# Kernel tuning notes

Measured on AMD Instinct MI355X. Metric: run time of the kernel, lower is better.

Reference implementation:

```python
import jax, jax.numpy as jnp
import numpy as np

N, E, D, G, OUT, K = 150000, 1200000, 128, 512, 2, 2
EPS = 1e-5


def setup_inputs() -> dict:
    key = jax.random.key(0)
    ks = jax.random.split(key, 8)
    nfeat = jax.random.normal(ks[0], (N, D), dtype=jnp.float32)
    src = jax.random.randint(ks[1], (E,), 0, N, dtype=jnp.int32)
    dst = jax.random.randint(ks[2], (E,), 0, N, dtype=jnp.int32)
    node2graph = jnp.sort(jax.random.randint(ks[3], (N,), 0, G, dtype=jnp.int32))
    s = 1.0 / np.sqrt(D)
    conv_w = jax.random.normal(ks[4], (D, D), dtype=jnp.float32) * s
    conv_b = jnp.zeros((D,), jnp.float32)
    gamma1 = jnp.ones((D,), jnp.float32)
    beta1 = jnp.zeros((D,), jnp.float32)
    gamma2 = jnp.ones((D,), jnp.float32)
    beta2 = jnp.zeros((D,), jnp.float32)
    pred_w = jax.random.normal(ks[5], (D, OUT), dtype=jnp.float32) * s
    pred_b = jnp.zeros((OUT,), jnp.float32)
    return {"nfeat": nfeat, "src": src, "dst": dst, "node2graph": node2graph,
            "num_graphs": G,
            "conv_w": conv_w, "conv_b": conv_b,
            "gamma1": gamma1, "beta1": beta1,
            "gamma2": gamma2, "beta2": beta2,
            "pred_w": pred_w, "pred_b": pred_b}


def _batchnorm(h, gamma, beta):
    # batch-norm over the node dimension (training-mode stats)
    mu = jnp.mean(h, axis=0)
    var = jnp.mean(jnp.square(h - mu), axis=0)
    return (h - mu) * jax.lax.rsqrt(var + EPS) * gamma + beta


def reference(nfeat, src, dst, node2graph, num_graphs,
              conv_w, conv_b, gamma1, beta1, gamma2, beta2, pred_w, pred_b):
    n = nfeat.shape[0]
    # symmetric degree normalization D^{-1/2} A D^{-1/2}
    deg = jax.ops.segment_sum(jnp.ones_like(dst, dtype=nfeat.dtype), dst, num_segments=n)
    dnorm = jax.lax.rsqrt(jnp.clip(deg, 1.0, None))  # [N]
    h = nfeat  # dropout with p=0 is identity
    for _ in range(K):  # k-hop SGC propagation interleaved with norm
        m = (h * dnorm[:, None])[src]                       # [E, D] gather
        h = jax.ops.segment_sum(m, dst, num_segments=n)     # scatter-add
        h = h * dnorm[:, None]
        h = _batchnorm(h, gamma1, beta1)
    h = h @ conv_w + conv_b          # SGConv linear
    h = _batchnorm(h, gamma2, beta2)  # middle norm
    h = jax.nn.relu(h)                # activation (dropout p=0)
    # mean pooling per graph
    cnt = jax.ops.segment_sum(jnp.ones((n,), h.dtype), node2graph, num_segments=num_graphs)
    g = jax.ops.segment_sum(h, node2graph, num_segments=num_graphs)
    g = g / jnp.clip(cnt, 1.0, None)[:, None]
    return g @ pred_w + pred_b  # [G, OUT]
```

## Files before the change

### kernel.cpp

```cpp
#include <hip/hip_runtime.h>
#include <hip/hip_fp16.h>
#include <cstddef>
#include <cstdint>

constexpr int DIMS = 128;
constexpr float BN_EPS = 1e-5f;
constexpr int NSH = 64;
constexpr int GB = 4096;
constexpr int NPB = 512;

typedef _Float16 f16x8 __attribute__((ext_vector_type(8)));
typedef float f32x4 __attribute__((ext_vector_type(4)));

static __device__ __forceinline__ f16x8 as_f16x8(uint4 u) {
  union { uint4 u; f16x8 h; } x; x.u = u; return x.h;
}
static __device__ __forceinline__ __half2 as_h2(uint32_t u) {
  union { uint32_t u; __half2 h; } x; x.u = u; return x.h;
}

__global__ void zero_k(float* __restrict__ fp, size_t nf) {
  size_t i = (size_t)blockIdx.x * blockDim.x + threadIdx.x;
  if (i < nf) fp[i] = 0.f;
}

__global__ void cvt_k(const float* __restrict__ in, uint32_t* __restrict__ out,
                      const float* __restrict__ dnorm, size_t n64) {
  size_t i = (size_t)blockIdx.x * blockDim.x + threadIdx.x;
  size_t stride = (size_t)gridDim.x * blockDim.x;
  const float2* in2 = (const float2*)in;
  for (; i < n64; i += stride) {
    float d = dnorm[i >> 6];
    float2 v = in2[i];
    __half2 h = __floats2half2_rn(v.x * d, v.y * d);
    out[i] = *(const uint32_t*)&h;
  }
}


__global__ __launch_bounds__(256) void cnt_k(const int* __restrict__ dst,
                                             int* __restrict__ C, int e, int chunk) {
  __shared__ int hist[512];
  int b = blockIdx.x;
  for (int j = threadIdx.x; j < 512; j += 256) hist[j] = 0;
  __syncthreads();
  int i0 = b * chunk;
  int i1 = i0 + chunk; if (i1 > e) i1 = e;
  for (int i = i0 + threadIdx.x; i < i1; i += 256)
    atomicAdd(&hist[dst[i] >> 9], 1);
  __syncthreads();
  for (int j = threadIdx.x; j < 512; j += 256) C[b * 512 + j] = hist[j];
}

__global__ __launch_bounds__(512) void colscan_k(int* __restrict__ C, int* __restrict__ tot) {
  int j = blockIdx.x;
  int t = threadIdx.x;
  int v = C[t * 512 + j];
  __shared__ int lds[512];
  lds[t] = v; __syncthreads();
  for (int off = 1; off < 512; off <<= 1) {
    int add = (t >= off) ? lds[t - off] : 0;
    __syncthreads();
    lds[t] += add;
    __syncthreads();
  }
  C[t * 512 + j] = lds[t] - v;
  if (t == 511) tot[j] = lds[511];
}

__global__ __launch_bounds__(512) void bscan_k(const int* __restrict__ tot, int nbins,
                                               int* __restrict__ boff, int e) {
  int t = threadIdx.x;
  int v = tot[t];
  __shared__ int lds[512];
  lds[t] = v; __syncthreads();
  for (int off = 1; off < 512; off <<= 1) {
    int add = (t >= off) ? lds[t - off] : 0;
    __syncthreads();
    lds[t] += add;
    __syncthreads();
  }
  boff[t] = lds[t] - v;
  if (t == 0) boff[nbins] = e;
}

__global__ __launch_bounds__(256) void scat_k(const int* __restrict__ src,
                                              const int* __restrict__ dst,
                                              const int* __restrict__ C,
                                              const int* __restrict__ boff,
                                              int* __restrict__ ebin, int e, int chunk) {
  __shared__ int cur[512];
  int b = blockIdx.x;
  for (int j = threadIdx.x; j < 512; j += 256) cur[j] = boff[j] + C[b * 512 + j];
  __syncthreads();
  int i0 = b * chunk;
  int i1 = i0 + chunk; if (i1 > e) i1 = e;
  for (int i = i0 + threadIdx.x; i < i1; i += 256) {
    int d = dst[i];
    int bin = d >> 9;
    int p = atomicAdd(&cur[bin], 1);
    ebin[p] = (src[i] << 9) | (d & 511);
  }
}

__global__ __launch_bounds__(512) void binidx_k(
    const int* __restrict__ ebin, const int* __restrict__ boff,
    int* __restrict__ row_off, float* __restrict__ dnorm, int n, int nbins) {
  __shared__ int cnt[512];
  __shared__ int scn[512];
  int b = blockIdx.x;
  int t = threadIdx.x;
  cnt[t] = 0;
  __syncthreads();
  int j0 = boff[b], j1 = boff[b + 1];
  for (int i = j0 + t; i < j1; i += 512) atomicAdd(&cnt[ebin[i] & 511], 1);
  __syncthreads();
  int v = cnt[t];
  scn[t] = v; __syncthreads();
  for (int off = 1; off < 512; off <<= 1) {
    int add = (t >= off) ? scn[t - off] : 0;
    __syncthreads();
    scn[t] += add;
    __syncthreads();
  }
  int node = (b << 9) + t;
  if (node < n) {
    row_off[node] = j0 + scn[t] - v;
    dnorm[node] = rsqrtf(fmaxf((float)v, 1.0f));
  }
  if (b == nbins - 1 && t == 0) row_off[n] = j1;
}

__global__ __launch_bounds__(512) void adj_bins_k(
    const int* __restrict__ ebin, const int* __restrict__ boff,
    const int* __restrict__ row_off, const float* __restrict__ dnorm,
    int* __restrict__ adj, float* __restrict__ wsum, int n) {
  __shared__ int cur[512];
  __shared__ int ro[512];
  __shared__ float ws[512];
  int b = blockIdx.x;
  int base = b << 9;
  int t = threadIdx.x;
  {
    cur[t] = 0;
    ws[t] = 0.f;
    int node = base + t;
    ro[t] = (node < n) ? row_off[node] : 0;
  }
  __syncthreads();
  int j0 = boff[b], j1 = boff[b + 1];
  for (int i = j0 + t; i < j1; i += 512) {
    int pk = ebin[i];
    int dl = pk & 511;
    int s = pk >> 9;
    int p = atomicAdd(&cur[dl], 1);
    adj[ro[dl] + p] = s;
    atomicAdd(&ws[dl], dnorm[s]);
  }
  __syncthreads();
  {
    int node = base + t;
    if (node < n) wsum[node] = ws[t];
  }
}

template <bool AFF>
__global__ __launch_bounds__(256) void gather_k(
    const uint32_t* __restrict__ Xu, uint32_t* __restrict__ Yout,
    const int* __restrict__ row_off, const int* __restrict__ adj,
    const float* __restrict__ dn, const float* __restrict__ wsum,
    const float* __restrict__ a, const float* __restrict__ b,
    float* __restrict__ sumS, float* __restrict__ sqS, int n, int nwaves) {
  int tid = threadIdx.x;
  int l = tid & 63, w = tid >> 6;
  int wid = blockIdx.x * 4 + w;
  uint32_t lu = (uint32_t)l;
  int f0 = 2 * l;
  float af0 = 1.f, bf0 = 0.f, af1 = 1.f, bf1 = 0.f;
  if (AFF) { af0 = a[f0]; bf0 = b[f0]; af1 = a[f0 + 1]; bf1 = b[f0 + 1]; }
  float s0 = 0.f, s1 = 0.f, q0 = 0.f, q1 = 0.f;

  for (int nodeA = wid; nodeA < n; nodeA += 2 * nwaves) {
    const int nodeB = nodeA + nwaves;
    const bool hasB = nodeB < n;
    int ja = row_off[nodeA];
    const int ea = row_off[nodeA + 1];
    int jb = hasB ? row_off[nodeB] : 0;
    const int eb = hasB ? row_off[nodeB + 1] : 0;
    float accA0 = 0.f, accA1 = 0.f, accB0 = 0.f, accB1 = 0.f;

    while ((ja < ea) || (jb < eb)) {
      uint32_t xa[8], xb[8];
      const bool runA = ja < ea, runB = jb < eb;
      if (runA) {
#pragma unroll
        for (int t = 0; t < 8; ++t) {
          int jj = ja + t;
          int jc = jj < ea ? jj : ea - 1;
          uint32_t sj = (uint32_t)adj[jc];
          uint32_t v = Xu[(sj << 6) + lu];
          xa[t] = (jj < ea) ? v : 0u;
        }
      }
      if (runB) {
#pragma unroll
        for (int t = 0; t < 8; ++t) {
          int jj = jb + t;
          int jc = jj < eb ? jj : eb - 1;
          uint32_t sj = (uint32_t)adj[jc];
          uint32_t v = Xu[(sj << 6) + lu];
          xb[t] = (jj < eb) ? v : 0u;
        }
      }
      if (runA) {
        __half2 t0 = __hadd2(as_h2(xa[0]), as_h2(xa[1]));
        __half2 t1 = __hadd2(as_h2(xa[2]), as_h2(xa[3]));
        __half2 t2 = __hadd2(as_h2(xa[4]), as_h2(xa[5]));
        __half2 t3 = __hadd2(as_h2(xa[6]), as_h2(xa[7]));
        float2 u0 = __half22float2(__hadd2(t0, t1));
        float2 u1 = __half22float2(__hadd2(t2, t3));
        accA0 += u0.x + u1.x;
        accA1 += u0.y + u1.y;
        ja += 8;
      }
      if (runB) {
        __half2 t0 = __hadd2(as_h2(xb[0]), as_h2(xb[1]));
        __half2 t1 = __hadd2(as_h2(xb[2]), as_h2(xb[3]));
        __half2 t2 = __hadd2(as_h2(xb[4]), as_h2(xb[5]));
        __half2 t3 = __hadd2(as_h2(xb[6]), as_h2(xb[7]));
        float2 u0 = __half22float2(__hadd2(t0, t1));
        float2 u1 = __half22float2(__hadd2(t2, t3));
        accB0 += u0.x + u1.x;
        accB1 += u0.y + u1.y;
        jb += 8;
      }
    }

    {
      float dnn = dn[nodeA];
      float v0, v1;
      if constexpr (AFF) {
        float wsn = wsum[nodeA];
        v0 = dnn * fmaf(af0, accA0, bf0 * wsn);
        v1 = dnn * fmaf(af1, accA1, bf1 * wsn);
        __half2 hv = __floats2half2_rn(v0, v1);
        Yout[((uint32_t)nodeA << 6) + lu] = *(const uint32_t*)&hv;
      } else {
        v0 = dnn * accA0;
        v1 = dnn * accA1;
        __half2 hv = __floats2half2_rn(v0 * dnn, v1 * dnn);
        Yout[((uint32_t)nodeA << 6) + lu] = *(const uint32_t*)&hv;
      }
      s0 += v0; s1 += v1; q0 += v0 * v0; q1 += v1 * v1;
    }
    if (hasB) {
      float dnn = dn[nodeB];
      float v0, v1;
      if constexpr (AFF) {
        float wsn = wsum[nodeB];
        v0 = dnn * fmaf(af0, accB0, bf0 * wsn);
        v1 = dnn * fmaf(af1, accB1, bf1 * wsn);
        __half2 hv = __floats2half2_rn(v0, v1);
        Yout[((uint32_t)nodeB << 6) + lu] = *(const uint32_t*)&hv;
      } else {
        v0 = dnn * accB0;
        v1 = dnn * accB1;
        __half2 hv = __floats2half2_rn(v0 * dnn, v1 * dnn);
        Yout[((uint32_t)nodeB << 6) + lu] = *(const uint32_t*)&hv;
      }
      s0 += v0; s1 += v1; q0 += v0 * v0; q1 += v1 * v1;
    }
  }

  __shared__ float red[4][256];
  red[w][l] = s0; red[w][64 + l] = s1; red[w][128 + l] = q0; red[w][192 + l] = q1;
  __syncthreads();
  float t = red[0][tid] + red[1][tid] + red[2][tid] + red[3][tid];
  int comp = tid >> 6, li = tid & 63;
  int sh = blockIdx.x & (NSH - 1);
  float* dstp = ((comp & 2) ? sqS : sumS) + sh * DIMS;
  atomicAdd(&dstp[2 * li + (comp & 1)], t);
}

__global__ void affine_k(const float* __restrict__ sum, const float* __restrict__ sq,
                         const float* __restrict__ gamma, const float* __restrict__ beta,
                         float* __restrict__ a, float* __restrict__ b, float invn) {
  int d = threadIdx.x;
  float s = 0.f, q = 0.f;
  for (int k = 0; k < NSH; ++k) { s += sum[k * DIMS + d]; q += sq[k * DIMS + d]; }
  float mu = s * invn;
  float var = q * invn - mu * mu;
  float rs = rsqrtf(var + BN_EPS);
  float ad = rs * gamma[d];
  a[d] = ad;
  b[d] = beta[d] - mu * ad;
}

__global__ void foldw_k(const float* __restrict__ W, const float* __restrict__ cb,
                        const float* __restrict__ a2, const float* __restrict__ b2,
                        __half* __restrict__ Wt, float* __restrict__ cp) {
  int o = blockIdx.x;
  int d = threadIdx.x;
  float w = W[d * DIMS + o];
  Wt[o * DIMS + d] = __float2half(a2[d] * w);
  __shared__ float red[128];
  red[d] = b2[d] * w;
  __syncthreads();
  for (int off = 64; off > 0; off >>= 1) {
    if (d < off) red[d] += red[d + off];
    __syncthreads();
  }
  if (d == 0) cp[o] = red[0] + cb[o];
}

__global__ __launch_bounds__(256) void matmul_k(
    const uint4* __restrict__ X, const uint4* __restrict__ Wt,
    const float* __restrict__ cp, uint4* __restrict__ Z,
    float* __restrict__ sumS, float* __restrict__ sqS, int n) {
  int tid = threadIdx.x;
  int l = tid & 63, w = tid >> 6;
  int rowg = l & 15;
  int kg = l >> 4;
  int r0 = (blockIdx.x * 4 + w) * 32;
  bool active = r0 < n;

  __shared__ __half outs[4][16][136];
  __shared__ float sred[4][128], qred[4][128];
  float svals[8], qvals[8];

  if (active) {
    f32x4 acc0[8] = {}, acc1[8] = {};
    const uint4* xr0 = X + (size_t)(r0 + rowg) * 16;
    const uint4* xr1 = X + (size_t)(r0 + 16 + rowg) * 16;
    bool ok0 = (r0 + rowg) < n;
    bool ok1 = (r0 + 16 + rowg) < n;
#pragma unroll
    for (int kk = 0; kk < 4; ++kk) {
      uint4 au0 = ok0 ? xr0[kk * 4 + kg] : make_uint4(0u, 0u, 0u, 0u);
      uint4 au1 = ok1 ? xr1[kk * 4 + kg] : make_uint4(0u, 0u, 0u, 0u);
      f16x8 a0 = as_f16x8(au0), a1 = as_f16x8(au1);
#pragma unroll
      for (int c = 0; c < 8; ++c) {
        f16x8 bfr = as_f16x8(Wt[(size_t)(c * 16 + rowg) * 16 + kk * 4 + kg]);
        acc0[c] = __builtin_amdgcn_mfma_f32_16x16x32_f16(a0, bfr, acc0[c], 0, 0, 0);
        acc1[c] = __builtin_amdgcn_mfma_f32_16x16x32_f16(a1, bfr, acc1[c], 0, 0, 0);
      }
    }
#pragma unroll
    for (int c = 0; c < 8; ++c) { svals[c] = 0.f; qvals[c] = 0.f; }
#pragma unroll
    for (int gidx = 0; gidx < 2; ++gidx) {
      int rbase = r0 + gidx * 16;
#pragma unroll
      for (int c = 0; c < 8; ++c) {
        float cpv = cp[c * 16 + rowg];
        f32x4 av = (gidx == 0) ? acc0[c] : acc1[c];
#pragma unroll
        for (int r = 0; r < 4; ++r) {
          int row = rbase + kg * 4 + r;
          float vv = av[r] + cpv;
          vv = (row < n) ? vv : 0.f;
          svals[c] += vv; qvals[c] += vv * vv;
          outs[w][kg * 4 + r][c * 16 + rowg] = __float2half(vv);
        }
      }
#pragma unroll
      for (int it = 0; it < 4; ++it) {
        int lr = it * 4 + kg;
        int grow = rbase + lr;
        if (grow < n)
          Z[(size_t)grow * 16 + rowg] = *(const uint4*)&outs[w][lr][rowg * 8];
      }
    }
#pragma unroll
    for (int c = 0; c < 8; ++c) {
      svals[c] += __shfl_xor(svals[c], 16); svals[c] += __shfl_xor(svals[c], 32);
      qvals[c] += __shfl_xor(qvals[c], 16); qvals[c] += __shfl_xor(qvals[c], 32);
    }
  }
  if (active) {
    if (kg == 0) {
#pragma unroll
      for (int c = 0; c < 8; ++c) {
        sred[w][c * 16 + rowg] = svals[c];
        qred[w][c * 16 + rowg] = qvals[c];
      }
    }
  } else {
    sred[w][l] = 0.f; sred[w][64 + l] = 0.f;
    qred[w][l] = 0.f; qred[w][64 + l] = 0.f;
  }
  __syncthreads();
  int f = tid & 127;
  int sh = blockIdx.x & (NSH - 1);
  if (tid < 128) {
    float s = sred[0][f] + sred[1][f] + sred[2][f] + sred[3][f];
    atomicAdd(&sumS[sh * DIMS + f], s);
  } else {
    float q = qred[0][f] + qred[1][f] + qred[2][f] + qred[3][f];
    atomicAdd(&sqS[sh * DIMS + f], q);
  }
}

__global__ void gstart_k(const int* __restrict__ n2g, int* __restrict__ gstart, int n, int G) {
  int i = blockIdx.x * blockDim.x + threadIdx.x;
  if (i >= n) return;
  int g = n2g[i];
  int gp = (i == 0) ? -1 : n2g[i - 1];
  for (int x = gp + 1; x <= g; ++x) gstart[x] = i;
  if (i == n - 1) {
    for (int x = g + 1; x <= G; ++x) gstart[x] = n;
  }
}

__global__ __launch_bounds__(512) void pool_pred_k(
    const uint4* __restrict__ Z, const int* __restrict__ gstart,
    const float* __restrict__ a3, const float* __restrict__ b3,
    const float* __restrict__ pw, const float* __restrict__ pb,
    float* __restrict__ out) {
  int g = blockIdx.x;
  int tid = threadIdx.x;
  int l = tid & 63, w = tid >> 6;
  int grp = l >> 4, fl = l & 15;
  int f0 = fl * 8;
  float av[8], bv[8];
#pragma unroll
  for (int q = 0; q < 8; ++q) { av[q] = a3[f0 + q]; bv[q] = b3[f0 + q]; }
  int s = gstart[g], e = gstart[g + 1];
  float rs[8] = {0.f, 0.f, 0.f, 0.f, 0.f, 0.f, 0.f, 0.f};
  for (int ni = s + (w * 4 + grp); ni < e; ni += 32) {
    uint4 zv = Z[(size_t)ni * 16 + fl];
    const __half2* h = (const __half2*)&zv;
#pragma unroll
    for (int q = 0; q < 4; ++q) {
      float2 z = __half22float2(h[q]);
      rs[2 * q] += fmaxf(fmaf(z.x, av[2 * q], bv[2 * q]), 0.f);
      rs[2 * q + 1] += fmaxf(fmaf(z.y, av[2 * q + 1], bv[2 * q + 1]), 0.f);
    }
  }
  float p0 = 0.f, p1 = 0.f;
#pragma unroll
  for (int q = 0; q < 8; ++q) {
    p0 += rs[q] * pw[(f0 + q) * 2 + 0];
    p1 += rs[q] * pw[(f0 + q) * 2 + 1];
  }
  __shared__ float r[2][512];
  r[0][tid] = p0; r[1][tid] = p1;
  __syncthreads();
  for (int off = 256; off > 0; off >>= 1) {
    if (tid < off) { r[0][tid] += r[0][tid + off]; r[1][tid] += r[1][tid + off]; }
    __syncthreads();
  }
  if (tid == 0) {
    float inv = 1.f / fmaxf((float)(e - s), 1.f);
    out[g * 2 + 0] = r[0][0] * inv + pb[0];
    out[g * 2 + 1] = r[1][0] * inv + pb[1];
  }
}

extern "C" void kernel_launch(void* const* d_in, const int* in_sizes, int n_in,
                              void* d_out, int out_size, void* d_ws, size_t ws_size,
                              hipStream_t stream) {
  const float* nfeat  = (const float*)d_in[0];
  const int*   src    = (const int*)d_in[1];
  const int*   dst    = (const int*)d_in[2];
  const int*   n2g    = (const int*)d_in[3];
  const float* conv_w = (const float*)d_in[5];
  const float* conv_b = (const float*)d_in[6];
  const float* gamma1 = (const float*)d_in[7];
  const float* beta1  = (const float*)d_in[8];
  const float* gamma2 = (const float*)d_in[9];
  const float* beta2  = (const float*)d_in[10];
  const float* pred_w = (const float*)d_in[11];
  const float* pred_b = (const float*)d_in[12];
  float* out = (float*)d_out;
  (void)n_in; (void)ws_size;

  const int n = in_sizes[0] / DIMS;
  const int e = in_sizes[1];
  const int g = out_size / 2;
  const int nbins = (n + 511) >> 9;

  char* p = (char*)d_ws;
  auto alloc = [&](size_t bytes) { char* r = p; p += (bytes + 255) & ~(size_t)255; return r; };
  uint32_t* Xp  = (uint32_t*)alloc((size_t)n * 64 * 4);
  uint32_t* W1  = (uint32_t*)alloc((size_t)n * 64 * 4);
  uint32_t* Y2  = (uint32_t*)alloc((size_t)n * 64 * 4);
  __half*   Zh  = (__half*)alloc((size_t)n * 64 * 4);
  float* dnorm = (float*)alloc((size_t)n * 4);
  float* stat  = (float*)alloc(((size_t)6 * NSH * DIMS + n) * 4);
  float* wsum  = stat + 6 * NSH * DIMS;
  float* affA  = (float*)alloc(3 * DIMS * 4);
  float* affB  = (float*)alloc(3 * DIMS * 4);
  __half* Wt   = (__half*)alloc(DIMS * DIMS * 2);
  float* cp    = (float*)alloc(DIMS * 4);
  int* row_off = (int*)alloc(((size_t)n + 1) * 4);
  int* adj     = (int*)alloc((size_t)e * 4);
  int* ebin    = (int*)alloc((size_t)e * 4);
  int* Cmat    = (int*)alloc((size_t)NPB * 512 * 4);
  int* tot     = (int*)alloc(512 * 4);
  int* boff    = (int*)alloc(520 * 4);
  int* gstart  = (int*)alloc(((size_t)g + 1) * 4);

  const int SLAB = NSH * DIMS;
  float* S0 = stat + 0 * SLAB; float* Q0 = stat + 1 * SLAB;
  float* S1 = stat + 2 * SLAB; float* Q1 = stat + 3 * SLAB;
  float* S2 = stat + 4 * SLAB; float* Q2 = stat + 5 * SLAB;

  const float invn = 1.0f / (float)n;
  const int nwaves = GB * 4;
  const int chunk = (e + NPB - 1) / NPB;

  zero_k<<<dim3(((size_t)6 * SLAB + 255) / 256), dim3(256), 0, stream>>>(stat, (size_t)6 * SLAB);
  cnt_k<<<dim3(NPB), dim3(256), 0, stream>>>(dst, Cmat, e, chunk);
  colscan_k<<<dim3(512), dim3(512), 0, stream>>>(Cmat, tot);
  bscan_k<<<dim3(1), dim3(512), 0, stream>>>(tot, nbins, boff, e);
  scat_k<<<dim3(NPB), dim3(256), 0, stream>>>(src, dst, Cmat, boff, ebin, e, chunk);
  binidx_k<<<dim3(nbins), dim3(512), 0, stream>>>(ebin, boff, row_off, dnorm, n, nbins);
  cvt_k<<<dim3(2048), dim3(256), 0, stream>>>(nfeat, Xp, dnorm, (size_t)n * 64);
  adj_bins_k<<<dim3(nbins), dim3(512), 0, stream>>>(ebin, boff, row_off, dnorm, adj, wsum, n);

  gather_k<false><<<dim3(GB), dim3(256), 0, stream>>>(
      Xp, W1, row_off, adj, dnorm, wsum, nullptr, nullptr, S0, Q0, n, nwaves);
  affine_k<<<dim3(1), dim3(DIMS), 0, stream>>>(S0, Q0, gamma1, beta1, affA + 0, affB + 0, invn);
  gather_k<true><<<dim3(GB), dim3(256), 0, stream>>>(
      W1, Y2, row_off, adj, dnorm, wsum, affA + 0, affB + 0, S1, Q1, n, nwaves);
  affine_k<<<dim3(1), dim3(DIMS), 0, stream>>>(S1, Q1, gamma1, beta1, affA + DIMS, affB + DIMS, invn);
  foldw_k<<<dim3(DIMS), dim3(DIMS), 0, stream>>>(conv_w, conv_b, affA + DIMS, affB + DIMS, Wt, cp);
  matmul_k<<<dim3((n + 127) / 128), dim3(256), 0, stream>>>(
      (const uint4*)Y2, (const uint4*)Wt, cp, (uint4*)Zh, S2, Q2, n);
  affine_k<<<dim3(1), dim3(DIMS), 0, stream>>>(S2, Q2, gamma2, beta2, affA + 2 * DIMS, affB + 2 * DIMS, invn);
  gstart_k<<<dim3((n + 255) / 256), dim3(256), 0, stream>>>(n2g, gstart, n, g);
  pool_pred_k<<<dim3(g), dim3(512), 0, stream>>>((const uint4*)Zh, gstart,
                                                 affA + 2 * DIMS, affB + 2 * DIMS,
                                                 pred_w, pred_b, out);
}
```

Baseline: 255.8 us.

## Vectorize conversion, pad adjacency to drop clamps, widen scatter blocks, halve gather grid

The fp32-to-fp16 conversion now reads float4 and writes uint2 instead of float2 and uint32. The adjacency array is padded with 8 zeroed entries, so the gather loop drops its per-element index clamp. The scatter kernel moves to 512 threads per block, one counter per thread. The gather grid is halved to 2048 blocks, which changes how many nodes each wave handles and the per-block stat reduction granularity.

```diff
diff --git a/kernel.cpp b/kernel.cpp
--- a/kernel.cpp
+++ b/kernel.cpp
@@ -6,7 +6,7 @@
 constexpr int DIMS = 128;
 constexpr float BN_EPS = 1e-5f;
 constexpr int NSH = 64;
-constexpr int GB = 4096;
+constexpr int GB = 2048;
 constexpr int NPB = 512;
 
 typedef _Float16 f16x8 __attribute__((ext_vector_type(8)));
@@ -17,6 +17,9 @@
 }
 static __device__ __forceinline__ __half2 as_h2(uint32_t u) {
   union { uint32_t u; __half2 h; } x; x.u = u; return x.h;
+}
+static __device__ __forceinline__ uint32_t h2bits(__half2 h) {
+  union { __half2 h; uint32_t u; } x; x.h = h; return x.u;
 }
 
 __global__ void zero_k(float* __restrict__ fp, size_t nf) {
@@ -24,16 +27,16 @@
   if (i < nf) fp[i] = 0.f;
 }
 
-__global__ void cvt_k(const float* __restrict__ in, uint32_t* __restrict__ out,
-                      const float* __restrict__ dnorm, size_t n64) {
+__global__ void cvt_k(const float4* __restrict__ in4, uint2* __restrict__ out,
+                      const float* __restrict__ dnorm, size_t n32) {
   size_t i = (size_t)blockIdx.x * blockDim.x + threadIdx.x;
   size_t stride = (size_t)gridDim.x * blockDim.x;
-  const float2* in2 = (const float2*)in;
-  for (; i < n64; i += stride) {
-    float d = dnorm[i >> 6];
-    float2 v = in2[i];
-    __half2 h = __floats2half2_rn(v.x * d, v.y * d);
-    out[i] = *(const uint32_t*)&h;
+  for (; i < n32; i += stride) {
+    float d = dnorm[i >> 5];
+    float4 v = in4[i];
+    __half2 h0 = __floats2half2_rn(v.x * d, v.y * d);
+    __half2 h1 = __floats2half2_rn(v.z * d, v.w * d);
+    out[i] = make_uint2(h2bits(h0), h2bits(h1));
   }
 }
 
@@ -69,7 +72,8 @@
 }
 
 __global__ __launch_bounds__(512) void bscan_k(const int* __restrict__ tot, int nbins,
-                                               int* __restrict__ boff, int e) {
+                                               int* __restrict__ boff, int* __restrict__ adj,
+                                               int e) {
   int t = threadIdx.x;
   int v = tot[t];
   __shared__ int lds[512];
@@ -82,20 +86,22 @@
   }
   boff[t] = lds[t] - v;
   if (t == 0) boff[nbins] = e;
-}
-
-__global__ __launch_bounds__(256) void scat_k(const int* __restrict__ src,
+  if (t < 8) adj[e + t] = 0;
+}
+
+__global__ __launch_bounds__(512) void scat_k(const int* __restrict__ src,
                                               const int* __restrict__ dst,
                                               const int* __restrict__ C,
                                               const int* __restrict__ boff,
                                               int* __restrict__ ebin, int e, int chunk) {
   __shared__ int cur[512];
   int b = blockIdx.x;
-  for (int j = threadIdx.x; j < 512; j += 256) cur[j] = boff[j] + C[b * 512 + j];
+  int t = threadIdx.x;
+  cur[t] = boff[t] + C[b * 512 + t];
   __syncthreads();
   int i0 = b * chunk;
   int i1 = i0 + chunk; if (i1 > e) i1 = e;
-  for (int i = i0 + threadIdx.x; i < i1; i += 256) {
+  for (int i = i0 + t; i < i1; i += 512) {
     int d = dst[i];
     int bin = d >> 9;
     int p = atomicAdd(&cur[bin], 1);
@@ -196,8 +202,7 @@
 #pragma unroll
         for (int t = 0; t < 8; ++t) {
           int jj = ja + t;
-          int jc = jj < ea ? jj : ea - 1;
-          uint32_t sj = (uint32_t)adj[jc];
+          uint32_t sj = (uint32_t)adj[jj];
           uint32_t v = Xu[(sj << 6) + lu];
           xa[t] = (jj < ea) ? v : 0u;
         }
@@ -206,8 +211,7 @@
 #pragma unroll
         for (int t = 0; t < 8; ++t) {
           int jj = jb + t;
-          int jc = jj < eb ? jj : eb - 1;
-          uint32_t sj = (uint32_t)adj[jc];
+          uint32_t sj = (uint32_t)adj[jj];
           uint32_t v = Xu[(sj << 6) + lu];
           xb[t] = (jj < eb) ? v : 0u;
         }
@@ -244,12 +248,12 @@
         v0 = dnn * fmaf(af0, accA0, bf0 * wsn);
         v1 = dnn * fmaf(af1, accA1, bf1 * wsn);
         __half2 hv = __floats2half2_rn(v0, v1);
-        Yout[((uint32_t)nodeA << 6) + lu] = *(const uint32_t*)&hv;
+        Yout[((uint32_t)nodeA << 6) + lu] = h2bits(hv);
       } else {
         v0 = dnn * accA0;
         v1 = dnn * accA1;
         __half2 hv = __floats2half2_rn(v0 * dnn, v1 * dnn);
-        Yout[((uint32_t)nodeA << 6) + lu] = *(const uint32_t*)&hv;
+        Yout[((uint32_t)nodeA << 6) + lu] = h2bits(hv);
       }
       s0 += v0; s1 += v1; q0 += v0 * v0; q1 += v1 * v1;
     }
@@ -261,12 +265,12 @@
         v0 = dnn * fmaf(af0, accB0, bf0 * wsn);
         v1 = dnn * fmaf(af1, accB1, bf1 * wsn);
         __half2 hv = __floats2half2_rn(v0, v1);
-        Yout[((uint32_t)nodeB << 6) + lu] = *(const uint32_t*)&hv;
+        Yout[((uint32_t)nodeB << 6) + lu] = h2bits(hv);
       } else {
         v0 = dnn * accB0;
         v1 = dnn * accB1;
         __half2 hv = __floats2half2_rn(v0 * dnn, v1 * dnn);
-        Yout[((uint32_t)nodeB << 6) + lu] = *(const uint32_t*)&hv;
+        Yout[((uint32_t)nodeB << 6) + lu] = h2bits(hv);
       }
       s0 += v0; s1 += v1; q0 += v0 * v0; q1 += v1 * v1;
     }
@@ -495,7 +499,7 @@
   __half* Wt   = (__half*)alloc(DIMS * DIMS * 2);
   float* cp    = (float*)alloc(DIMS * 4);
   int* row_off = (int*)alloc(((size_t)n + 1) * 4);
-  int* adj     = (int*)alloc((size_t)e * 4);
+  int* adj     = (int*)alloc(((size_t)e + 8) * 4);
   int* ebin    = (int*)alloc((size_t)e * 4);
   int* Cmat    = (int*)alloc((size_t)NPB * 512 * 4);
   int* tot     = (int*)alloc(512 * 4);
@@ -514,10 +518,11 @@
   zero_k<<<dim3(((size_t)6 * SLAB + 255) / 256), dim3(256), 0, stream>>>(stat, (size_t)6 * SLAB);
   cnt_k<<<dim3(NPB), dim3(256), 0, stream>>>(dst, Cmat, e, chunk);
   colscan_k<<<dim3(512), dim3(512), 0, stream>>>(Cmat, tot);
-  bscan_k<<<dim3(1), dim3(512), 0, stream>>>(tot, nbins, boff, e);
-  scat_k<<<dim3(NPB), dim3(256), 0, stream>>>(src, dst, Cmat, boff, ebin, e, chunk);
+  bscan_k<<<dim3(1), dim3(512), 0, stream>>>(tot, nbins, boff, adj, e);
+  scat_k<<<dim3(NPB), dim3(512), 0, stream>>>(src, dst, Cmat, boff, ebin, e, chunk);
   binidx_k<<<dim3(nbins), dim3(512), 0, stream>>>(ebin, boff, row_off, dnorm, n, nbins);
-  cvt_k<<<dim3(2048), dim3(256), 0, stream>>>(nfeat, Xp, dnorm, (size_t)n * 64);
+  cvt_k<<<dim3(2048), dim3(256), 0, stream>>>((const float4*)nfeat, (uint2*)Xp, dnorm,
+                                              (size_t)n * 32);
   adj_bins_k<<<dim3(nbins), dim3(512), 0, stream>>>(ebin, boff, row_off, dnorm, adj, wsum, n);
 
   gather_k<false><<<dim3(GB), dim3(256), 0, stream>>>(
```

New measurement: 265.9 us. 1.04x slower.
